# Optimization experiments

Measured on AMD Instinct MI355X. Metric: run time of the kernel, lower is better.

The kernel has to match this reference:

```python
import jax, jax.numpy as jnp
import numpy as np

N = 50000      # nodes
E = 800000     # edges
D_DISC = 64
D_CONT = 13    # per-slice continuous features (39/3)
EMB = 256
HID = 512
SLOPE = 0.01   # torch leaky_relu default


def lrelu(x):
    return jax.nn.leaky_relu(x, SLOPE)


def gcn_conv(x, W, b, src, dst, n):
    """PyG GCNConv with add_self_loops=True (self loops appended by caller),
    symmetric normalization D^-1/2 A D^-1/2, bias."""
    x = x @ W                                   # [N, EMB]
    ones = jnp.ones(src.shape[0], x.dtype)
    deg = jax.ops.segment_sum(ones, dst, num_segments=n)   # in-degree incl self loop
    dinv = jax.lax.rsqrt(jnp.maximum(deg, 1e-12))
    norm = dinv[src] * dinv[dst]                # [E+N]
    out = jax.ops.segment_sum(x[src] * norm[:, None], dst, num_segments=n)
    return out + b


def setup_inputs() -> dict:
    key = jax.random.key(0)
    ks = jax.random.split(key, 24)
    def lin(k, fan_in, fan_out):
        bound = 1.0 / np.sqrt(fan_in)
        k1, k2 = jax.random.split(k)
        W = jax.random.uniform(k1, (fan_in, fan_out), jnp.float32, -bound, bound)
        b = jax.random.uniform(k2, (fan_out,), jnp.float32, -bound, bound)
        return W, b
    Wd, bd = lin(ks[0], D_DISC, EMB)
    Wc1, bc1 = lin(ks[1], D_CONT, EMB)
    Wc2, bc2 = lin(ks[2], D_CONT, EMB)
    Wg0, bg0 = lin(ks[3], D_DISC, EMB)
    Wg1, bg1 = lin(ks[4], EMB, EMB)
    Wg2, bg2 = lin(ks[5], EMB, EMB)
    Wf, bf = lin(ks[6], 4 * EMB, HID)
    Wl1, bl1 = lin(ks[7], HID, HID // 2)
    Wl2, bl2 = lin(ks[8], HID // 2, 1)
    discrete_x = jax.random.normal(ks[9], (N, D_DISC), jnp.float32)
    continous_x = jax.random.normal(ks[10], (N, 3 * D_CONT), jnp.float32)
    edge_index = jax.random.randint(ks[11], (2, E), 0, N, jnp.int64)
    return {
        'discrete_x': discrete_x, 'continous_x': continous_x,
        'Wd': Wd, 'bd': bd, 'Wc1': Wc1, 'bc1': bc1, 'Wc2': Wc2, 'bc2': bc2,
        'Wg0': Wg0, 'bg0': bg0, 'Wg1': Wg1, 'bg1': bg1, 'Wg2': Wg2, 'bg2': bg2,
        'Wf': Wf, 'bf': bf, 'Wl1': Wl1, 'bl1': bl1, 'Wl2': Wl2, 'bl2': bl2,
        'edge_index': edge_index,
    }


def reference(discrete_x, continous_x, Wd, bd, Wc1, bc1, Wc2, bc2,
              Wg0, bg0, Wg1, bg1, Wg2, bg2, Wf, bf, Wl1, bl1, Wl2, bl2,
              edge_index):
    n = discrete_x.shape[0]
    loop = jnp.arange(n, dtype=edge_index.dtype)
    src = jnp.concatenate([edge_index[0], loop])
    dst = jnp.concatenate([edge_index[1], loop])

    x_d = lrelu(discrete_x @ Wd + bd)
    x_c1 = lrelu(continous_x[:, :13] @ Wc1 + bc1)
    x_c2 = lrelu(continous_x[:, 13:26] @ Wc2 + bc2)
    x_g = lrelu(discrete_x @ Wg0 + bg0)
    x_g = lrelu(gcn_conv(x_g, Wg1, bg1, src, dst, n))
    x_g = lrelu(gcn_conv(x_g, Wg2, bg2, src, dst, n))

    h_ci = lrelu(jnp.concatenate([x_d, x_c1, x_c2, x_g], axis=1) @ Wf + bf)
    s = lrelu(h_ci @ Wl1 + bl1)
    # dropout: eval mode (training=False) -> identity
    s_ci = jax.nn.sigmoid((s @ Wl2 + bl2)).squeeze()
    return (s_ci, s_ci, s_ci, h_ci, h_ci)
```

## Files before the change

### kernel.cpp

```cpp
#include <hip/hip_runtime.h>
#include <math.h>

#define NNODES 50000
#define NEDGES 800000
#define EMB 256
#define HID 512


typedef __bf16 bf16x8 __attribute__((ext_vector_type(8)));
typedef float f32x4 __attribute__((ext_vector_type(4)));
typedef unsigned short us4v __attribute__((ext_vector_type(4)));
typedef unsigned short us8v __attribute__((ext_vector_type(8)));

__device__ __forceinline__ unsigned short f2bf(float x) {
    unsigned int u = __float_as_uint(x);
    u += 0x7FFF + ((u >> 16) & 1);
    return (unsigned short)(u >> 16);
}

__device__ __forceinline__ f32x4 mfma_bf16(us8v a, us8v b, f32x4 c) {
    return __builtin_amdgcn_mfma_f32_16x16x32_bf16(
        __builtin_bit_cast(bf16x8, a), __builtin_bit_cast(bf16x8, b), c, 0, 0, 0);
}

__global__ void wsplit(const float* __restrict__ W, int K, int N,
                       unsigned short* __restrict__ th, unsigned short* __restrict__ tl)
{
    int idx = blockIdx.x * 256 + threadIdx.x;
    if (idx >= K * N) return;
    int n = idx / K, k = idx - n * K;
    float x = W[(size_t)k * N + n];
    unsigned short h = f2bf(x);
    float hf = __uint_as_float((unsigned int)h << 16);
    th[idx] = h;
    tl[idx] = f2bf(x - hf);
}

__global__ __launch_bounds__(256) void gemm_mfma(
    const float* __restrict__ A, int lda,
    const unsigned short* __restrict__ BTh, const unsigned short* __restrict__ BTl,
    float* __restrict__ C, int ldc, float* __restrict__ C2,
    const float* __restrict__ bias, int M, int N, int K, int act)
{
    __shared__ unsigned short AsH[128 * 64];
    __shared__ unsigned short AsL[128 * 64];
    const int bm = blockIdx.y * 128;
    const int bn = blockIdx.x * 128;
    const int tid = threadIdx.x;
    const int lane = tid & 63;
    const int wid = tid >> 6;
    const int wm = wid >> 1, wn = wid & 1;
    const int l15 = lane & 15, l4 = lane >> 4;

    f32x4 acc[4][4] = {};

    for (int k0 = 0; k0 < K; k0 += 64) {
#pragma unroll
        for (int u = 0; u < 8; ++u) {
            int fid = tid + u * 256;
            int m = fid >> 4;
            int j4 = fid & 15;
            int gr = bm + m;
            float4 v = make_float4(0.f, 0.f, 0.f, 0.f);
            if (gr < M) v = *(const float4*)(A + (size_t)gr * lda + k0 + j4 * 4);
            float e[4] = {v.x, v.y, v.z, v.w};
            us4v h, l;
#pragma unroll
            for (int t = 0; t < 4; ++t) {
                unsigned short hh = f2bf(e[t]);
                h[t] = hh;
                l[t] = f2bf(e[t] - __uint_as_float((unsigned int)hh << 16));
            }
            int phys = m * 64 + ((((j4 >> 1)) ^ (m & 7)) << 3) + (j4 & 1) * 4;
            *(us4v*)&AsH[phys] = h;
            *(us4v*)&AsL[phys] = l;
        }
        __syncthreads();

#pragma unroll
        for (int ks = 0; ks < 2; ++ks) {
            us8v ah[4], al[4];
            int kb = ks * 4 + l4;
#pragma unroll
            for (int fi = 0; fi < 4; ++fi) {
                int row = wm * 64 + fi * 16 + l15;
                int phys = row * 64 + ((kb ^ (row & 7)) << 3);
                ah[fi] = *(const us8v*)&AsH[phys];
                al[fi] = *(const us8v*)&AsL[phys];
            }
            size_t kg = (size_t)(k0 + ks * 32 + l4 * 8);
#pragma unroll
            for (int fj = 0; fj < 4; ++fj) {
                int col = bn + wn * 64 + fj * 16 + l15;
                size_t boff = (size_t)col * (size_t)K + kg;
                us8v bh = *(const us8v*)&BTh[boff];
                us8v bl = *(const us8v*)&BTl[boff];
#pragma unroll
                for (int fi = 0; fi < 4; ++fi) {
                    acc[fi][fj] = mfma_bf16(ah[fi], bh, acc[fi][fj]);
                    acc[fi][fj] = mfma_bf16(al[fi], bh, acc[fi][fj]);
                    acc[fi][fj] = mfma_bf16(ah[fi], bl, acc[fi][fj]);
                }
            }
        }
        __syncthreads();
    }

    float bs[4];
#pragma unroll
    for (int fj = 0; fj < 4; ++fj)
        bs[fj] = bias ? bias[bn + wn * 64 + fj * 16 + l15] : 0.f;

#pragma unroll
    for (int fi = 0; fi < 4; ++fi) {
#pragma unroll
        for (int r = 0; r < 4; ++r) {
            int row = bm + wm * 64 + fi * 16 + l4 * 4 + r;
            if (row >= M) continue;
#pragma unroll
            for (int fj = 0; fj < 4; ++fj) {
                int col = bn + wn * 64 + fj * 16 + l15;
                float v = acc[fi][fj][r] + bs[fj];
                if (act) v = v > 0.f ? v : 0.01f * v;
                C[(size_t)row * ldc + col] = v;
                if (C2) C2[(size_t)row * ldc + col] = v;
            }
        }
    }
}

#define BM 128
#define BN 128
#define BK 16

__global__ __launch_bounds__(256) void gemm_kernel(
    const float* __restrict__ A, int lda,
    const float* __restrict__ B, int ldb,
    float* __restrict__ C, int ldc,
    float* __restrict__ C2,
    const float* __restrict__ bias,
    int M, int N, int K, int act)
{
    __shared__ float As[BK][BM];
    __shared__ float Bs[BK][BN];
    const int bm = blockIdx.y * BM;
    const int bn = blockIdx.x * BN;
    const int tid = threadIdx.x;
    const int tx = tid & 15;
    const int ty = tid >> 4;

    const bool avec = ((((uintptr_t)A) & 15) == 0) && ((lda & 3) == 0);

    float acc[8][8] = {};

    for (int k0 = 0; k0 < K; k0 += BK) {
        if (avec) {
#pragma unroll
            for (int it = 0; it < 2; ++it) {
                int aid = tid + it * 256;
                int m = aid >> 2;
                int kq = aid & 3;
                int gr = bm + m;
                int gk = k0 + kq * 4;
                float4 v = {0.f, 0.f, 0.f, 0.f};
                if (gr < M) {
                    if (gk + 3 < K) {
                        v = *(const float4*)(A + (size_t)gr * lda + gk);
                    } else {
                        float t0 = (gk + 0 < K) ? A[(size_t)gr * lda + gk + 0] : 0.f;
                        float t1 = (gk + 1 < K) ? A[(size_t)gr * lda + gk + 1] : 0.f;
                        float t2 = (gk + 2 < K) ? A[(size_t)gr * lda + gk + 2] : 0.f;
                        float t3 = (gk + 3 < K) ? A[(size_t)gr * lda + gk + 3] : 0.f;
                        v = make_float4(t0, t1, t2, t3);
                    }
                }
                int k = kq * 4;
                As[k + 0][m ^ (((k + 0) & 7) << 2)] = v.x;
                As[k + 1][m ^ (((k + 1) & 7) << 2)] = v.y;
                As[k + 2][m ^ (((k + 2) & 7) << 2)] = v.z;
                As[k + 3][m ^ (((k + 3) & 7) << 2)] = v.w;
            }
        } else {
            for (int l = tid; l < BM * BK; l += 256) {
                int m = l >> 4;
                int k = l & 15;
                int gr = bm + m, gc = k0 + k;
                float v = (gr < M && gc < K) ? A[(size_t)gr * lda + gc] : 0.f;
                As[k][m ^ ((k & 7) << 2)] = v;
            }
        }
#pragma unroll
        for (int it = 0; it < 2; ++it) {
            int fid = tid + it * 256;
            int k = fid >> 5;
            int n4 = fid & 31;
            int gk = k0 + k;
            int gn = bn + n4 * 4;
            float4 v = {0.f, 0.f, 0.f, 0.f};
            if (gk < K) {
                if (gn + 3 < N) {
                    v = *(const float4*)(B + (size_t)gk * ldb + gn);
                } else {
                    float t0 = (gn + 0 < N) ? B[(size_t)gk * ldb + gn + 0] : 0.f;
                    float t1 = (gn + 1 < N) ? B[(size_t)gk * ldb + gn + 1] : 0.f;
                    float t2 = (gn + 2 < N) ? B[(size_t)gk * ldb + gn + 2] : 0.f;
                    float t3 = (gn + 3 < N) ? B[(size_t)gk * ldb + gn + 3] : 0.f;
                    v = make_float4(t0, t1, t2, t3);
                }
            }
            *(float4*)&Bs[k][n4 * 4] = v;
        }
        __syncthreads();

#pragma unroll
        for (int k = 0; k < BK; ++k) {
            const int sw = (k & 7) << 2;
            float4 a0 = *(const float4*)&As[k][(ty * 4) ^ sw];
            float4 a1 = *(const float4*)&As[k][(ty * 4 + 64) ^ sw];
            float4 b0 = *(const float4*)&Bs[k][tx * 4];
            float4 b1 = *(const float4*)&Bs[k][tx * 4 + 64];
            float av[8] = {a0.x, a0.y, a0.z, a0.w, a1.x, a1.y, a1.z, a1.w};
            float bv[8] = {b0.x, b0.y, b0.z, b0.w, b1.x, b1.y, b1.z, b1.w};
#pragma unroll
            for (int i = 0; i < 8; ++i)
#pragma unroll
                for (int j = 0; j < 8; ++j)
                    acc[i][j] += av[i] * bv[j];
        }
        __syncthreads();
    }

#pragma unroll
    for (int i = 0; i < 8; ++i) {
        int r = bm + ((i >> 2) * 64) + ty * 4 + (i & 3);
        if (r >= M) continue;
#pragma unroll
        for (int jh = 0; jh < 2; ++jh) {
            int c0 = bn + jh * 64 + tx * 4;
            if (c0 + 3 < N) {
                float v0 = acc[i][jh * 4 + 0];
                float v1 = acc[i][jh * 4 + 1];
                float v2 = acc[i][jh * 4 + 2];
                float v3 = acc[i][jh * 4 + 3];
                if (bias) {
                    v0 += bias[c0 + 0]; v1 += bias[c0 + 1];
                    v2 += bias[c0 + 2]; v3 += bias[c0 + 3];
                }
                if (act) {
                    v0 = v0 > 0.f ? v0 : 0.01f * v0;
                    v1 = v1 > 0.f ? v1 : 0.01f * v1;
                    v2 = v2 > 0.f ? v2 : 0.01f * v2;
                    v3 = v3 > 0.f ? v3 : 0.01f * v3;
                }
                float4 pack = make_float4(v0, v1, v2, v3);
                *(float4*)(C + (size_t)r * ldc + c0) = pack;
                if (C2) *(float4*)(C2 + (size_t)r * ldc + c0) = pack;
            } else {
#pragma unroll
                for (int e = 0; e < 4; ++e) {
                    int c = c0 + e;
                    if (c >= N) continue;
                    float v = acc[i][jh * 4 + e];
                    if (bias) v += bias[c];
                    if (act) v = v > 0.f ? v : 0.01f * v;
                    C[(size_t)r * ldc + c] = v;
                    if (C2) C2[(size_t)r * ldc + c] = v;
                }
            }
        }
    }
}

__global__ void count_deg(const int* __restrict__ dst, int* __restrict__ deg, int nE)
{
    int e = blockIdx.x * 256 + threadIdx.x;
    if (e < nE) atomicAdd(&deg[dst[e]], 1);
}

__global__ void dinv_kernel(const int* __restrict__ deg, float* __restrict__ dinv, int n)
{
    int i = blockIdx.x * 256 + threadIdx.x;
    if (i < n) dinv[i] = rsqrtf((float)deg[i] + 1.0f);
}

__global__ __launch_bounds__(256) void scan1(const int* __restrict__ deg,
                                             int* __restrict__ excl,
                                             int* __restrict__ blocksum, int n)
{
    __shared__ int tsum[256];
    int base = blockIdx.x * 1024;
    int t = threadIdx.x;
    int v[4], s = 0;
#pragma unroll
    for (int j = 0; j < 4; ++j) {
        int idx = base + t * 4 + j;
        v[j] = (idx < n) ? deg[idx] : 0;
        s += v[j];
    }
    tsum[t] = s;
    __syncthreads();
    for (int off = 1; off < 256; off <<= 1) {
        int x = (t >= off) ? tsum[t - off] : 0;
        __syncthreads();
        tsum[t] += x;
        __syncthreads();
    }
    int toff = tsum[t] - s;
    int run = 0;
#pragma unroll
    for (int j = 0; j < 4; ++j) {
        int idx = base + t * 4 + j;
        if (idx < n) excl[idx] = toff + run;
        run += v[j];
    }
    if (t == 255) blocksum[blockIdx.x] = tsum[255];
}

__global__ void scan2(int* __restrict__ blocksum, int nb)
{
    if (threadIdx.x == 0 && blockIdx.x == 0) {
        int run = 0;
        for (int i = 0; i < nb; ++i) {
            int v = blocksum[i];
            blocksum[i] = run;
            run += v;
        }
    }
}

__global__ void scan3(int* __restrict__ rowptr, int* __restrict__ cursor,
                      const int* __restrict__ excl, const int* __restrict__ blocksum, int n)
{
    int idx = blockIdx.x * 256 + threadIdx.x;
    if (idx < n) {
        int v = excl[idx] + blocksum[idx >> 10];
        rowptr[idx] = v;
        cursor[idx] = v;
    }
    if (idx == 0) rowptr[n] = NEDGES;
}

__global__ void fill_csr(const int* __restrict__ src, const int* __restrict__ dst,
                         const float* __restrict__ dinv, int* __restrict__ cursor,
                         int* __restrict__ src_sorted, float* __restrict__ w_sorted, int nE)
{
    int e = blockIdx.x * 256 + threadIdx.x;
    if (e >= nE) return;
    int s = src[e], d = dst[e];
    int pos = atomicAdd(&cursor[d], 1);
    src_sorted[pos] = s;
    w_sorted[pos] = dinv[s] * dinv[d];
}

__global__ __launch_bounds__(256) void gather_conv(
    const float* __restrict__ t, const int* __restrict__ rowptr,
    const int* __restrict__ src_sorted, const float* __restrict__ w_sorted,
    const float* __restrict__ dinv, const float* __restrict__ bias,
    float* __restrict__ out, int ldc)
{
    int node = blockIdx.x * 4 + (threadIdx.x >> 6);
    if (node >= NNODES) return;
    int lane = threadIdx.x & 63;
    int p0 = rowptr[node], p1 = rowptr[node + 1];
    const float4* tv = (const float4*)t;
    float4 acc = {0.f, 0.f, 0.f, 0.f};
    for (int p = p0; p < p1; ++p) {
        int s = src_sorted[p];
        float w = w_sorted[p];
        float4 v = tv[(size_t)s * 64 + lane];
        acc.x += v.x * w; acc.y += v.y * w; acc.z += v.z * w; acc.w += v.w * w;
    }
    float di = dinv[node];
    float w2 = di * di;
    float4 self = tv[(size_t)node * 64 + lane];
    float4 b = ((const float4*)bias)[lane];
    acc.x += self.x * w2 + b.x;
    acc.y += self.y * w2 + b.y;
    acc.z += self.z * w2 + b.z;
    acc.w += self.w * w2 + b.w;
    acc.x = acc.x > 0.f ? acc.x : 0.01f * acc.x;
    acc.y = acc.y > 0.f ? acc.y : 0.01f * acc.y;
    acc.z = acc.z > 0.f ? acc.z : 0.01f * acc.z;
    acc.w = acc.w > 0.f ? acc.w : 0.01f * acc.w;
    *((float4*)(out + (size_t)node * ldc) + lane) = acc;
}

__global__ __launch_bounds__(256) void rowdot_sigmoid(
    const float* __restrict__ s, const float* __restrict__ w, const float* __restrict__ b,
    float* __restrict__ out, int n)
{
    int row = blockIdx.x * 4 + (threadIdx.x >> 6);
    int lane = threadIdx.x & 63;
    if (row >= n) return;
    const float4* sr = (const float4*)(s + (size_t)row * 256);
    const float4* wr = (const float4*)w;
    float4 a = sr[lane], c = wr[lane];
    float p = a.x * c.x + a.y * c.y + a.z * c.z + a.w * c.w;
#pragma unroll
    for (int off = 32; off > 0; off >>= 1) p += __shfl_down(p, off);
    if (lane == 0) {
        float v = 1.0f / (1.0f + expf(-(p + b[0])));
        out[row] = v;
        out[n + row] = v;
        out[2 * n + row] = v;
    }
}

extern "C" void kernel_launch(void* const* d_in, const int* in_sizes, int n_in,
                              void* d_out, int out_size, void* d_ws, size_t ws_size,
                              hipStream_t stream)
{
    const float* discrete_x = (const float*)d_in[0];
    const float* continous_x = (const float*)d_in[1];
    const float* Wd  = (const float*)d_in[2];  const float* bd  = (const float*)d_in[3];
    const float* Wc1 = (const float*)d_in[4];  const float* bc1 = (const float*)d_in[5];
    const float* Wc2 = (const float*)d_in[6];  const float* bc2 = (const float*)d_in[7];
    const float* Wg0 = (const float*)d_in[8];  const float* bg0 = (const float*)d_in[9];
    const float* Wg1 = (const float*)d_in[10]; const float* bg1 = (const float*)d_in[11];
    const float* Wg2 = (const float*)d_in[12]; const float* bg2 = (const float*)d_in[13];
    const float* Wf  = (const float*)d_in[14]; const float* bf  = (const float*)d_in[15];
    const float* Wl1 = (const float*)d_in[16]; const float* bl1 = (const float*)d_in[17];
    const float* Wl2 = (const float*)d_in[18]; const float* bl2 = (const float*)d_in[19];
    const int* edge_index = (const int*)d_in[20];
    const int* src = edge_index;
    const int* dst = edge_index + NEDGES;

    float* out = (float*)d_out;
    float* ws = (float*)d_ws;

    float* dinv       = ws;
    int*   deg        = (int*)(ws + 50048);
    int*   rowptr     = (int*)(ws + 2 * 50048);
    int*   cursor     = (int*)(ws + 3 * 50048 + 64);
    int*   excl       = (int*)(ws + 4 * 50048 + 64);
    int*   blocksum   = (int*)(ws + 5 * 50048 + 64);
    int*   src_sorted = (int*)(ws + 5 * 50048 + 128);
    float* w_sorted   = ws + 5 * 50048 + 128 + NEDGES;
    float* xcat       = w_sorted + NEDGES;
    float* xg         = xcat + (size_t)NNODES * 1024;
    float* tbuf       = xg   + (size_t)NNODES * EMB;
    float* sbuf       = tbuf + (size_t)NNODES * EMB;

    float* h_out  = out + 3 * (size_t)NNODES;
    float* h_out2 = h_out + (size_t)NNODES * HID;

    unsigned short* wl1_h = (unsigned short*)out;
    unsigned short* wl1_l = wl1_h + 512 * 256;
    unsigned short* wd_h  = (unsigned short*)h_out2;
    unsigned short* wd_l  = wd_h  + 64 * 256;
    unsigned short* wg0_h = wd_l  + 64 * 256;
    unsigned short* wg0_l = wg0_h + 64 * 256;
    unsigned short* wg1_h = wg0_l + 64 * 256;
    unsigned short* wg1_l = wg1_h + 256 * 256;
    unsigned short* wg2_h = wg1_l + 256 * 256;
    unsigned short* wg2_l = wg2_h + 256 * 256;
    unsigned short* wf_h  = (unsigned short*)sbuf;
    unsigned short* wf_l  = wf_h + 1024 * 512;

    dim3 blk(256);
    auto gemmF = [&](const float* A, int lda, const float* B, int ldb, float* C, int ldc,
                     float* C2, const float* bias, int M, int N, int K, int act) {
        dim3 grid((N + BN - 1) / BN, (M + BM - 1) / BM);
        hipLaunchKernelGGL(gemm_kernel, grid, blk, 0, stream,
                           A, lda, B, ldb, C, ldc, C2, bias, M, N, K, act);
    };
    auto gemmM = [&](const float* A, int lda, const unsigned short* th, const unsigned short* tl,
                     float* C, int ldc, float* C2, const float* bias,
                     int M, int N, int K, int act) {
        dim3 grid(N / 128, (M + 127) / 128);
        hipLaunchKernelGGL(gemm_mfma, grid, blk, 0, stream,
                           A, lda, th, tl, C, ldc, C2, bias, M, N, K, act);
    };
    auto wsp = [&](const float* W, int K, int N, unsigned short* th, unsigned short* tl) {
        hipLaunchKernelGGL(wsplit, dim3((K * N + 255) / 256), blk, 0, stream, W, K, N, th, tl);
    };

    wsp(Wd,  64,   256, wd_h,  wd_l);
    wsp(Wg0, 64,   256, wg0_h, wg0_l);
    wsp(Wg1, 256,  256, wg1_h, wg1_l);
    wsp(Wg2, 256,  256, wg2_h, wg2_l);
    wsp(Wf,  1024, 512, wf_h,  wf_l);
    wsp(Wl1, 512,  256, wl1_h, wl1_l);

    hipMemsetAsync(deg, 0, NNODES * sizeof(int), stream);
    hipLaunchKernelGGL(count_deg, dim3((NEDGES + 255) / 256), blk, 0, stream, dst, deg, NEDGES);
    hipLaunchKernelGGL(dinv_kernel, dim3((NNODES + 255) / 256), blk, 0, stream, deg, dinv, NNODES);
    int nb = (NNODES + 1023) / 1024;
    hipLaunchKernelGGL(scan1, dim3(nb), blk, 0, stream, deg, excl, blocksum, NNODES);
    hipLaunchKernelGGL(scan2, dim3(1), blk, 0, stream, blocksum, nb);
    hipLaunchKernelGGL(scan3, dim3((NNODES + 255) / 256), blk, 0, stream,
                       rowptr, cursor, excl, blocksum, NNODES);
    hipLaunchKernelGGL(fill_csr, dim3((NEDGES + 255) / 256), blk, 0, stream,
                       src, dst, dinv, cursor, src_sorted, w_sorted, NEDGES);

    gemmM(discrete_x, 64, wd_h, wd_l, xcat + 0, 1024, nullptr, bd, NNODES, 256, 64, 1);
    gemmF(continous_x,      39, Wc1, EMB, xcat + 256, 1024, nullptr, bc1, NNODES, EMB, 13, 1);
    gemmF(continous_x + 13, 39, Wc2, EMB, xcat + 512, 1024, nullptr, bc2, NNODES, EMB, 13, 1);
    gemmM(discrete_x, 64, wg0_h, wg0_l, xg, EMB, nullptr, bg0, NNODES, 256, 64, 1);

    gemmM(xg, EMB, wg1_h, wg1_l, tbuf, EMB, nullptr, nullptr, NNODES, 256, 256, 0);
    hipLaunchKernelGGL(gather_conv, dim3((NNODES + 3) / 4), blk, 0, stream,
                       tbuf, rowptr, src_sorted, w_sorted, dinv, bg1, xg, EMB);

    gemmM(xg, EMB, wg2_h, wg2_l, tbuf, EMB, nullptr, nullptr, NNODES, 256, 256, 0);
    hipLaunchKernelGGL(gather_conv, dim3((NNODES + 3) / 4), blk, 0, stream,
                       tbuf, rowptr, src_sorted, w_sorted, dinv, bg2, xcat + 768, 1024);

    gemmM(xcat, 1024, wf_h, wf_l, h_out, HID, h_out2, bf, NNODES, 512, 1024, 1);

    gemmM(h_out, HID, wl1_h, wl1_l, sbuf, 256, nullptr, bl1, NNODES, 256, 512, 1);

    hipLaunchKernelGGL(rowdot_sigmoid, dim3((NNODES + 3) / 4), blk, 0, stream,
                       sbuf, Wl2, bl2, out, NNODES);
}
```

Before: 1.519 ms.

## Double-buffer A tile in LDS and prefetch next K-slice into registers

The GEMM kernel now keeps two LDS buffers for the split-bf16 A tile and loads the next 64-wide K slice of A into registers while the current slice is being consumed. This drops the second barrier per iteration and hides global load latency behind MFMA work. B fragment loads are batched ahead of the MFMA loop and address arithmetic is hoisted out of it. The cost is doubled LDS use and more live registers, which may reduce occupancy.

```diff
diff --git a/kernel.cpp b/kernel.cpp
--- a/kernel.cpp
+++ b/kernel.cpp
@@ -42,8 +42,8 @@
     float* __restrict__ C, int ldc, float* __restrict__ C2,
     const float* __restrict__ bias, int M, int N, int K, int act)
 {
-    __shared__ unsigned short AsH[128 * 64];
-    __shared__ unsigned short AsL[128 * 64];
+    __shared__ unsigned short AsH[2][128 * 64];
+    __shared__ unsigned short AsL[2][128 * 64];
     const int bm = blockIdx.y * 128;
     const int bn = blockIdx.x * 128;
     const int tid = threadIdx.x;
@@ -52,58 +52,90 @@
     const int wm = wid >> 1, wn = wid & 1;
     const int l15 = lane & 15, l4 = lane >> 4;
 
+    int smidx[8], sj4[8];
+    const float* sptr[8];
+#pragma unroll
+    for (int u = 0; u < 8; ++u) {
+        int fid = tid + u * 256;
+        int m = fid >> 4;
+        int j4 = fid & 15;
+        smidx[u] = m;
+        sj4[u] = j4;
+        int gr = bm + m;
+        sptr[u] = (gr < M) ? (A + (size_t)gr * lda + j4 * 4) : nullptr;
+    }
+
+    const unsigned short* bhp[4];
+    const unsigned short* blp[4];
+#pragma unroll
+    for (int fj = 0; fj < 4; ++fj) {
+        size_t coff = (size_t)(bn + wn * 64 + fj * 16 + l15) * (size_t)K;
+        bhp[fj] = BTh + coff;
+        blp[fj] = BTl + coff;
+    }
+
     f32x4 acc[4][4] = {};
-
-    for (int k0 = 0; k0 < K; k0 += 64) {
+    float4 pref[8];
+
+    const int nk = K >> 6;
+
+#pragma unroll
+    for (int u = 0; u < 8; ++u)
+        pref[u] = sptr[u] ? *(const float4*)(sptr[u]) : make_float4(0.f, 0.f, 0.f, 0.f);
+
+    for (int t = 0; t < nk; ++t) {
+        const int cur = t & 1;
 #pragma unroll
         for (int u = 0; u < 8; ++u) {
-            int fid = tid + u * 256;
-            int m = fid >> 4;
-            int j4 = fid & 15;
-            int gr = bm + m;
-            float4 v = make_float4(0.f, 0.f, 0.f, 0.f);
-            if (gr < M) v = *(const float4*)(A + (size_t)gr * lda + k0 + j4 * 4);
-            float e[4] = {v.x, v.y, v.z, v.w};
+            float e[4] = {pref[u].x, pref[u].y, pref[u].z, pref[u].w};
             us4v h, l;
 #pragma unroll
-            for (int t = 0; t < 4; ++t) {
-                unsigned short hh = f2bf(e[t]);
-                h[t] = hh;
-                l[t] = f2bf(e[t] - __uint_as_float((unsigned int)hh << 16));
-            }
+            for (int q = 0; q < 4; ++q) {
+                unsigned short hh = f2bf(e[q]);
+                h[q] = hh;
+                l[q] = f2bf(e[q] - __uint_as_float((unsigned int)hh << 16));
+            }
+            int m = smidx[u], j4 = sj4[u];
             int phys = m * 64 + ((((j4 >> 1)) ^ (m & 7)) << 3) + (j4 & 1) * 4;
-            *(us4v*)&AsH[phys] = h;
-            *(us4v*)&AsL[phys] = l;
+            *(us4v*)&AsH[cur][phys] = h;
+            *(us4v*)&AsL[cur][phys] = l;
+        }
+        if (t + 1 < nk) {
+            const int koff = (t + 1) * 64;
+#pragma unroll
+            for (int u = 0; u < 8; ++u)
+                pref[u] = sptr[u] ? *(const float4*)(sptr[u] + koff)
+                                  : make_float4(0.f, 0.f, 0.f, 0.f);
         }
         __syncthreads();
 
+        const int k0 = t * 64;
 #pragma unroll
         for (int ks = 0; ks < 2; ++ks) {
-            us8v ah[4], al[4];
-            int kb = ks * 4 + l4;
+            us8v ah[4], al[4], bh[4], bl[4];
+            const int kb = ks * 4 + l4;
 #pragma unroll
             for (int fi = 0; fi < 4; ++fi) {
                 int row = wm * 64 + fi * 16 + l15;
                 int phys = row * 64 + ((kb ^ (row & 7)) << 3);
-                ah[fi] = *(const us8v*)&AsH[phys];
-                al[fi] = *(const us8v*)&AsL[phys];
-            }
-            size_t kg = (size_t)(k0 + ks * 32 + l4 * 8);
+                ah[fi] = *(const us8v*)&AsH[cur][phys];
+                al[fi] = *(const us8v*)&AsL[cur][phys];
+            }
+            const size_t kg = (size_t)(k0 + ks * 32 + l4 * 8);
 #pragma unroll
             for (int fj = 0; fj < 4; ++fj) {
-                int col = bn + wn * 64 + fj * 16 + l15;
-                size_t boff = (size_t)col * (size_t)K + kg;
-                us8v bh = *(const us8v*)&BTh[boff];
-                us8v bl = *(const us8v*)&BTl[boff];
+                bh[fj] = *(const us8v*)(bhp[fj] + kg);
+                bl[fj] = *(const us8v*)(blp[fj] + kg);
+            }
+#pragma unroll
+            for (int fj = 0; fj < 4; ++fj)
 #pragma unroll
                 for (int fi = 0; fi < 4; ++fi) {
-                    acc[fi][fj] = mfma_bf16(ah[fi], bh, acc[fi][fj]);
-                    acc[fi][fj] = mfma_bf16(al[fi], bh, acc[fi][fj]);
-                    acc[fi][fj] = mfma_bf16(ah[fi], bl, acc[fi][fj]);
+                    acc[fi][fj] = mfma_bf16(ah[fi], bh[fj], acc[fi][fj]);
+                    acc[fi][fj] = mfma_bf16(al[fi], bh[fj], acc[fi][fj]);
+                    acc[fi][fj] = mfma_bf16(ah[fi], bl[fj], acc[fi][fj]);
                 }
-            }
-        }
-        __syncthreads();
+        }
     }
 
     float bs[4];
```

New measurement: 1.310 ms. 13.7% less time.
